# Kernel tuning notes

Measured on AMD Instinct MI355X. Metric: run time of the kernel, lower is better.

Reference implementation:

```python
import jax, jax.numpy as jnp
import numpy as np

N_EMBEDDING = 32
HEAD_SIZE = 64
B, T = 8, 4096


def setup_inputs() -> dict:
    key = jax.random.key(0)
    kx, kk, kq, kv = jax.random.split(key, 4)
    x = jax.random.normal(kx, (B, T, N_EMBEDDING), dtype=jnp.float32)
    Wk = jax.random.normal(kk, (N_EMBEDDING, HEAD_SIZE), dtype=jnp.float32) * 0.05
    Wq = jax.random.normal(kq, (N_EMBEDDING, HEAD_SIZE), dtype=jnp.float32) * 0.05
    Wv = jax.random.normal(kv, (N_EMBEDDING, HEAD_SIZE), dtype=jnp.float32) * 0.05
    return {"x": x, "Wk": Wk, "Wq": Wq, "Wv": Wv}


def reference(x, Wk, Wq, Wv):
    # x: [B, T, C]; projections (no bias)
    k = jnp.einsum("btc,cd->btd", x, Wk)  # [B,T,D]
    q = jnp.einsum("btc,cd->btd", x, Wq)
    v = jnp.einsum("btc,cd->btd", x, Wv)
    # raw scores (NOTE: original module applies no 1/sqrt(D) scaling)
    wei = jnp.einsum("bqd,bkd->bqk", q, k)  # [B,T,T]
    t = x.shape[1]
    causal = jnp.tril(jnp.ones((t, t), dtype=bool))
    wei = jnp.where(causal[None, :, :], wei, -jnp.inf)
    wei = jax.nn.softmax(wei, axis=-1)
    out = jnp.einsum("bqk,bkd->bqd", wei, v)  # [B,T,D]
    return out
```

## Files before the change

### kernel.cpp

```cpp
#include <hip/hip_runtime.h>
#include <hip/hip_bf16.h>

constexpr int Bc = 8;
constexpr int Tt = 4096;
constexpr int Dd = 64;

typedef __attribute__((ext_vector_type(8))) short short8;
typedef __attribute__((ext_vector_type(4))) float floatx4;
typedef __attribute__((ext_vector_type(4))) __fp16 half4;
typedef __attribute__((ext_vector_type(2))) __fp16 half2v;
typedef uint4   __attribute__((may_alias)) uint4_a;
typedef short8  __attribute__((may_alias)) short8_a;
typedef ushort4 __attribute__((may_alias)) ushort4_a;
typedef float4  __attribute__((may_alias)) float4_a;
typedef half4   __attribute__((may_alias)) half4_a;

#define MFMA16(A, B, C)  __builtin_amdgcn_mfma_f32_16x16x32_bf16(A, B, C, 0, 0, 0)
#define MFMAH16(A, B, C) __builtin_amdgcn_mfma_f32_16x16x16f16(A, B, C, 0, 0, 0)
constexpr float LOG2E = 1.4426950408889634f;

__device__ __forceinline__ unsigned rnd16(float x) {
    unsigned u; __builtin_memcpy(&u, &x, 4); return u + 0x8000u;
}
__device__ __forceinline__ unsigned pk_bf2(float lo, float hi) {
    return __builtin_amdgcn_perm(rnd16(hi), rnd16(lo), 0x07060302);
}
__device__ __forceinline__ ushort4 pack4(floatx4 d) {
    union { unsigned u[2]; ushort4 v; } r;
    r.u[0] = pk_bf2(d[0], d[1]);
    r.u[1] = pk_bf2(d[2], d[3]);
    return r.v;
}
__device__ __forceinline__ short8 cvt8(float4 a, float4 b) {
    union { unsigned u[4]; short8 s; } r;
    r.u[0] = pk_bf2(a.x, a.y);
    r.u[1] = pk_bf2(a.z, a.w);
    r.u[2] = pk_bf2(b.x, b.y);
    r.u[3] = pk_bf2(b.z, b.w);
    return r.s;
}

__global__ __launch_bounds__(1024, 4) void attn_kernel(
    const float* __restrict__ x,
    const float* __restrict__ Wk, const float* __restrict__ Wq,
    const float* __restrict__ Wv,
    float* __restrict__ out)
{
    __shared__ uint4 sStage[4096];
    __shared__ uint4 sP[256];
    __shared__ uint4 sG[128];

    int b  = blockIdx.x & 7;
    int pr = blockIdx.x >> 3;
    int tid  = threadIdx.x;
    int wave = tid >> 6, lane = tid & 63;
    int group = wave >> 2, gw = wave & 3;
    int ln15 = lane & 15, quad = lane >> 4;
    size_t bT = (size_t)b * Tt;

    const int tg = tid & 255;
    const int srow = tg >> 2, scg = tg & 3;

    if (wave == 0) {
        floatx4 gC[2][2];
        #pragma unroll
        for (int mt = 0; mt < 2; ++mt)
            #pragma unroll
            for (int nt = 0; nt < 2; ++nt) gC[mt][nt] = (floatx4){0.f,0.f,0.f,0.f};
        #pragma unroll
        for (int kt = 0; kt < 2; ++kt) {
            short8 aG[2], bG[2];
            #pragma unroll
            for (int mt = 0; mt < 2; ++mt) {
                const float* qp = Wq + (ln15 + 16*mt)*64 + 32*kt + quad*8;
                float4 a = ((const float4_a*)qp)[0], bb = ((const float4_a*)qp)[1];
                a.x*=LOG2E; a.y*=LOG2E; a.z*=LOG2E; a.w*=LOG2E;
                bb.x*=LOG2E; bb.y*=LOG2E; bb.z*=LOG2E; bb.w*=LOG2E;
                aG[mt] = cvt8(a, bb);
                const float* kp = Wk + (ln15 + 16*mt)*64 + 32*kt + quad*8;
                bG[mt] = cvt8(((const float4_a*)kp)[0], ((const float4_a*)kp)[1]);
            }
            #pragma unroll
            for (int mt = 0; mt < 2; ++mt)
                #pragma unroll
                for (int nt = 0; nt < 2; ++nt)
                    gC[mt][nt] = MFMA16(aG[mt], bG[nt], gC[mt][nt]);
        }
        unsigned short* sGh = (unsigned short*)sG;
        #pragma unroll
        for (int mt = 0; mt < 2; ++mt)
            #pragma unroll
            for (int nt = 0; nt < 2; ++nt)
                *(ushort4_a*)(sGh + (16*nt + ln15)*32 + 16*mt + quad*4)
                    = pack4(gC[mt][nt]);
    }
    __syncthreads();

    const int gBase = group * 1024;
    unsigned short* sYh = (unsigned short*)sP;

    for (int phase = 0; phase < 2; ++phase) {
        const int qtP = phase ? pr : 63 - pr;
        const int q0 = qtP * 64;
        const int qrow = q0 + gw*16 + ln15;

        float4 pX0, pX1;
        if (group <= qtP) {
            const float* xp = x + (bT + group*64 + srow)*32 + scg*8;
            pX0 = ((const float4_a*)xp)[0];
            pX1 = ((const float4_a*)xp)[1];
        }

        if (wave < 8) {
            int qs = wave & 3, mt = wave >> 2;
            union { uint4 u; short8 s; } g;
            g.u = sG[(16*mt + ln15)*4 + quad];
            const float* xp = x + (bT + q0 + qs*16 + ln15)*32 + quad*8;
            short8 xq = cvt8(((const float4_a*)xp)[0], ((const float4_a*)xp)[1]);
            floatx4 d = (floatx4){0.f,0.f,0.f,0.f};
            d = MFMA16(g.s, xq, d);
            *(ushort4_a*)(sYh + (qs*16 + ln15)*32 + 16*mt + quad*4) = pack4(d);
        }
        __syncthreads();
        short8 bq;
        {
            union { uint4 u; short8 s; } t0;
            t0.u = sP[(gw*16 + ln15)*4 + quad];
            bq = t0.s;
        }

        floatx4 z4[2];
        z4[0] = (floatx4){0.f,0.f,0.f,0.f};
        z4[1] = (floatx4){0.f,0.f,0.f,0.f};
        float l_lane = 0.f;

        const int nIter = (qtP + 4) >> 2;

        for (int it = 0; it < nIter; ++it) {
            int kt = 4*it + group;
            bool active = (kt <= qtP);
            const int stB = gBase + (it & 1) * 512;
            if (active) {
                unsigned u0 = pk_bf2(pX0.x, pX0.y), u1 = pk_bf2(pX0.z, pX0.w);
                unsigned u2 = pk_bf2(pX1.x, pX1.y), u3 = pk_bf2(pX1.z, pX1.w);
                uint4 xu; xu.x = u0; xu.y = u1; xu.z = u2; xu.w = u3;
                sStage[stB + srow*4 + (scg ^ (srow & 3))] = xu;
                union { half2v h; unsigned short us[2]; } w01, w23, w45, w67;
                w01.h = __builtin_amdgcn_cvt_pkrtz(pX0.x, pX0.y);
                w23.h = __builtin_amdgcn_cvt_pkrtz(pX0.z, pX0.w);
                w45.h = __builtin_amdgcn_cvt_pkrtz(pX1.x, pX1.y);
                w67.h = __builtin_amdgcn_cvt_pkrtz(pX1.z, pX1.w);
                unsigned short hv[8] = { w01.us[0], w01.us[1], w23.us[0], w23.us[1],
                                         w45.us[0], w45.us[1], w67.us[0], w67.us[1] };
                unsigned short* sXh = (unsigned short*)(sStage + stB + 256);
                const int cb = scg * 8, gx = srow >> 2, ko = srow & 3;
                #pragma unroll
                for (int jj = 0; jj < 8; ++jj) {
                    int c = cb + jj;
                    sXh[c*64 + ((gx ^ (c & 15)) << 2) + ko] = hv[jj];
                }
            }
            __syncthreads();
            int ktn = kt + 4;
            if (ktn <= qtP) {
                const float* xp = x + (bT + ktn*64 + srow)*32 + scg*8;
                pX0 = ((const float4_a*)xp)[0];
                pX1 = ((const float4_a*)xp)[1];
            }
            if (!active) continue;
            int k0 = kt * 64;

            const int xsw = quad ^ (ln15 & 3);
            floatx4 s4[4];
            #pragma unroll
            for (int t = 0; t < 4; ++t) {
                union { uint4 u; short8 s; } a;
                a.u = sStage[stB + (16*t + ln15)*4 + xsw];
                floatx4 c = (floatx4){0.f,0.f,0.f,0.f};
                c = MFMA16(a.s, bq, c);
                s4[t] = c;
            }

            if (kt == qtP) {
                #pragma unroll
                for (int t = 0; t < 4; ++t) {
                    int keyb = k0 + 16*t + quad*4;
                    #pragma unroll
                    for (int r = 0; r < 4; ++r) {
                        float p = (keyb + r <= qrow) ? __builtin_amdgcn_exp2f(s4[t][r]) : 0.f;
                        s4[t][r] = p;
                        l_lane += p;
                    }
                }
            } else {
                #pragma unroll
                for (int t = 0; t < 4; ++t)
                    #pragma unroll
                    for (int r = 0; r < 4; ++r) {
                        float p = __builtin_amdgcn_exp2f(s4[t][r]);
                        s4[t][r] = p;
                        l_lane += p;
                    }
            }

            const unsigned short* sXh = (const unsigned short*)(sStage + stB + 256);
            #pragma unroll
            for (int t = 0; t < 4; ++t) {
                union { half2v h2[2]; half4 h4; } pb;
                pb.h2[0] = __builtin_amdgcn_cvt_pkrtz(s4[t][0], s4[t][1]);
                pb.h2[1] = __builtin_amdgcn_cvt_pkrtz(s4[t][2], s4[t][3]);
                const int gph = ((4*t + quad) ^ ln15) << 2;
                #pragma unroll
                for (int mt = 0; mt < 2; ++mt) {
                    half4 xa = *(const half4_a*)(sXh + (16*mt + ln15)*64 + gph);
                    z4[mt] = MFMAH16(xa, pb.h4, z4[mt]);
                }
            }
        }

        __syncthreads();
        int li = gw*64 + lane;
        ((float*)sP)[wave*64 + lane] = l_lane;
        if (group != 0) {
            float4* st = (float4*)(sStage + group*1024);
            st[li*2 + 0] = make_float4(z4[0][0], z4[0][1], z4[0][2], z4[0][3]);
            st[li*2 + 1] = make_float4(z4[1][0], z4[1][1], z4[1][2], z4[1][3]);
        }
        __syncthreads();
        if (group == 0) {
            short8 wv_f[4];
            #pragma unroll
            for (int t = 0; t < 4; ++t) {
                int col = 16*t + ln15;
                union { unsigned u[4]; short8 s; } rv;
                #pragma unroll
                for (int jj = 0; jj < 4; ++jj) {
                    const float* v0 = Wv + (quad*8 + 2*jj) * 64 + col;
                    rv.u[jj] = pk_bf2(v0[0], v0[64]);
                }
                wv_f[t] = rv.s;
            }
            float l = l_lane + ((float*)sP)[256 + li]
                    + ((float*)sP)[512 + li] + ((float*)sP)[768 + li];
            l += __shfl_xor(l, 16);
            l += __shfl_xor(l, 32);
            float inv = 1.f / l;
            #pragma unroll
            for (int g = 1; g < 4; ++g) {
                float4* st = (float4*)(sStage + g*1024);
                float4 a = st[li*2 + 0], bb = st[li*2 + 1];
                z4[0][0]+=a.x; z4[0][1]+=a.y; z4[0][2]+=a.z; z4[0][3]+=a.w;
                z4[1][0]+=bb.x; z4[1][1]+=bb.y; z4[1][2]+=bb.z; z4[1][3]+=bb.w;
            }
            unsigned short* sZb = (unsigned short*)sStage;
            #pragma unroll
            for (int mt = 0; mt < 2; ++mt)
                *(ushort4_a*)(sZb + (gw*16 + ln15)*32 + 16*mt + quad*4) = pack4(z4[mt]);
            union { uint4 u; short8 s; } zb;
            zb.u = sStage[(gw*16 + ln15)*4 + quad];
            #pragma unroll
            for (int t = 0; t < 4; ++t) {
                floatx4 o = (floatx4){0.f,0.f,0.f,0.f};
                o = MFMA16(wv_f[t], zb.s, o);
                *(float4_a*)(out + (bT + q0 + gw*16 + ln15)*Dd + 16*t + quad*4)
                    = make_float4(o[0]*inv, o[1]*inv, o[2]*inv, o[3]*inv);
            }
        }
        __syncthreads();
    }
}

extern "C" void kernel_launch(void* const* d_in, const int* in_sizes, int n_in,
                              void* d_out, int out_size, void* d_ws, size_t ws_size,
                              hipStream_t stream)
{
    const float* x  = (const float*)d_in[0];
    const float* Wk = (const float*)d_in[1];
    const float* Wq = (const float*)d_in[2];
    const float* Wv = (const float*)d_in[3];
    float* out = (float*)d_out;

    attn_kernel<<<Bc * 32, 1024, 0, stream>>>(x, Wk, Wq, Wv, out);
}
```

Measured before the change: 86.95 us.

## Process both paired query tiles in one key sweep sharing staged x tiles

Instead of two sequential phases (long tile 63-pr, then short tile pr), the kernel processes both query tiles in a single loop over key tiles, reusing each staged x tile for both score and PV MFMAs. This removes the second pass of x loading, conversion and LDS staging, along with the extra barriers, for the short tile. In exchange it raises register pressure from the doubled accumulators and score arrays, and it doubles the sP buffer.

After: 90.60 us. 4.2% more time.

```diff
diff --git a/kernel.cpp b/kernel.cpp
--- a/kernel.cpp
+++ b/kernel.cpp
@@ -47,11 +47,13 @@
     float* __restrict__ out)
 {
     __shared__ uint4 sStage[4096];
-    __shared__ uint4 sP[256];
+    __shared__ uint4 sP[512];
     __shared__ uint4 sG[128];
 
     int b  = blockIdx.x & 7;
     int pr = blockIdx.x >> 3;
+    const int qtA = 63 - pr, qtB = pr;
+    const int q0A = qtA * 64, q0B = qtB * 64;
     int tid  = threadIdx.x;
     int wave = tid >> 6, lane = tid & 63;
     int group = wave >> 2, gw = wave & 3;
@@ -99,97 +101,117 @@
     const int gBase = group * 1024;
     unsigned short* sYh = (unsigned short*)sP;
 
-    for (int phase = 0; phase < 2; ++phase) {
-        const int qtP = phase ? pr : 63 - pr;
-        const int q0 = qtP * 64;
-        const int qrow = q0 + gw*16 + ln15;
-
-        float4 pX0, pX1;
-        if (group <= qtP) {
-            const float* xp = x + (bT + group*64 + srow)*32 + scg*8;
+    float4 pX0, pX1;
+    {
+        const float* xp = x + (bT + group*64 + srow)*32 + scg*8;
+        pX0 = ((const float4_a*)xp)[0];
+        pX1 = ((const float4_a*)xp)[1];
+    }
+
+    {
+        int tileY = wave >> 3, qs = (wave >> 1) & 3, mt = wave & 1;
+        int q0Y = tileY ? q0B : q0A;
+        union { uint4 u; short8 s; } g;
+        g.u = sG[(16*mt + ln15)*4 + quad];
+        const float* xp = x + (bT + q0Y + qs*16 + ln15)*32 + quad*8;
+        short8 xq = cvt8(((const float4_a*)xp)[0], ((const float4_a*)xp)[1]);
+        floatx4 d = (floatx4){0.f,0.f,0.f,0.f};
+        d = MFMA16(g.s, xq, d);
+        *(ushort4_a*)(sYh + tileY*2048 + (qs*16 + ln15)*32 + 16*mt + quad*4)
+            = pack4(d);
+    }
+    __syncthreads();
+    short8 bqA, bqB;
+    {
+        union { uint4 u; short8 s; } t0, t1;
+        t0.u = sP[(gw*16 + ln15)*4 + quad];
+        t1.u = sP[256 + (gw*16 + ln15)*4 + quad];
+        bqA = t0.s; bqB = t1.s;
+    }
+
+    floatx4 z4A[2], z4B[2];
+    z4A[0] = (floatx4){0.f,0.f,0.f,0.f}; z4A[1] = z4A[0];
+    z4B[0] = z4A[0];                     z4B[1] = z4A[0];
+    float lA = 0.f, lB = 0.f;
+    const int qrowA = q0A + gw*16 + ln15;
+    const int qrowB = q0B + gw*16 + ln15;
+
+    const int nIter = (qtA + 4) >> 2;
+
+    for (int it = 0; it < nIter; ++it) {
+        int kt = 4*it + group;
+        bool activeA = (kt <= qtA);
+        const int stB = gBase + (it & 1) * 512;
+        if (activeA) {
+            unsigned u0 = pk_bf2(pX0.x, pX0.y), u1 = pk_bf2(pX0.z, pX0.w);
+            unsigned u2 = pk_bf2(pX1.x, pX1.y), u3 = pk_bf2(pX1.z, pX1.w);
+            uint4 xu; xu.x = u0; xu.y = u1; xu.z = u2; xu.w = u3;
+            sStage[stB + srow*4 + (scg ^ (srow & 3))] = xu;
+            union { half2v h; unsigned short us[2]; } w01, w23, w45, w67;
+            w01.h = __builtin_amdgcn_cvt_pkrtz(pX0.x, pX0.y);
+            w23.h = __builtin_amdgcn_cvt_pkrtz(pX0.z, pX0.w);
+            w45.h = __builtin_amdgcn_cvt_pkrtz(pX1.x, pX1.y);
+            w67.h = __builtin_amdgcn_cvt_pkrtz(pX1.z, pX1.w);
+            unsigned short hv[8] = { w01.us[0], w01.us[1], w23.us[0], w23.us[1],
+                                     w45.us[0], w45.us[1], w67.us[0], w67.us[1] };
+            unsigned short* sXh = (unsigned short*)(sStage + stB + 256);
+            const int cb = scg * 8, gx = srow >> 2, ko = srow & 3;
+            #pragma unroll
+            for (int jj = 0; jj < 8; ++jj) {
+                int c = cb + jj;
+                sXh[c*64 + ((gx ^ (c & 15)) << 2) + ko] = hv[jj];
+            }
+        }
+        __syncthreads();
+        int ktn = kt + 4;
+        if (ktn <= qtA) {
+            const float* xp = x + (bT + ktn*64 + srow)*32 + scg*8;
             pX0 = ((const float4_a*)xp)[0];
             pX1 = ((const float4_a*)xp)[1];
         }
-
-        if (wave < 8) {
-            int qs = wave & 3, mt = wave >> 2;
-            union { uint4 u; short8 s; } g;
-            g.u = sG[(16*mt + ln15)*4 + quad];
-            const float* xp = x + (bT + q0 + qs*16 + ln15)*32 + quad*8;
-            short8 xq = cvt8(((const float4_a*)xp)[0], ((const float4_a*)xp)[1]);
-            floatx4 d = (floatx4){0.f,0.f,0.f,0.f};
-            d = MFMA16(g.s, xq, d);
-            *(ushort4_a*)(sYh + (qs*16 + ln15)*32 + 16*mt + quad*4) = pack4(d);
-        }
-        __syncthreads();
-        short8 bq;
-        {
-            union { uint4 u; short8 s; } t0;
-            t0.u = sP[(gw*16 + ln15)*4 + quad];
-            bq = t0.s;
-        }
-
-        floatx4 z4[2];
-        z4[0] = (floatx4){0.f,0.f,0.f,0.f};
-        z4[1] = (floatx4){0.f,0.f,0.f,0.f};
-        float l_lane = 0.f;
-
-        const int nIter = (qtP + 4) >> 2;
-
-        for (int it = 0; it < nIter; ++it) {
-            int kt = 4*it + group;
-            bool active = (kt <= qtP);
-            const int stB = gBase + (it & 1) * 512;
-            if (active) {
-                unsigned u0 = pk_bf2(pX0.x, pX0.y), u1 = pk_bf2(pX0.z, pX0.w);
-                unsigned u2 = pk_bf2(pX1.x, pX1.y), u3 = pk_bf2(pX1.z, pX1.w);
-                uint4 xu; xu.x = u0; xu.y = u1; xu.z = u2; xu.w = u3;
-                sStage[stB + srow*4 + (scg ^ (srow & 3))] = xu;
-                union { half2v h; unsigned short us[2]; } w01, w23, w45, w67;
-                w01.h = __builtin_amdgcn_cvt_pkrtz(pX0.x, pX0.y);
-                w23.h = __builtin_amdgcn_cvt_pkrtz(pX0.z, pX0.w);
-                w45.h = __builtin_amdgcn_cvt_pkrtz(pX1.x, pX1.y);
-                w67.h = __builtin_amdgcn_cvt_pkrtz(pX1.z, pX1.w);
-                unsigned short hv[8] = { w01.us[0], w01.us[1], w23.us[0], w23.us[1],
-                                         w45.us[0], w45.us[1], w67.us[0], w67.us[1] };
-                unsigned short* sXh = (unsigned short*)(sStage + stB + 256);
-                const int cb = scg * 8, gx = srow >> 2, ko = srow & 3;
-                #pragma unroll
-                for (int jj = 0; jj < 8; ++jj) {
-                    int c = cb + jj;
-                    sXh[c*64 + ((gx ^ (c & 15)) << 2) + ko] = hv[jj];
+        if (!activeA) continue;
+        int k0 = kt * 64;
+        bool doB = (kt <= qtB);
+
+        const int xsw = quad ^ (ln15 & 3);
+        floatx4 sA[4], sB[4];
+        #pragma unroll
+        for (int t = 0; t < 4; ++t) {
+            union { uint4 u; short8 s; } a;
+            a.u = sStage[stB + (16*t + ln15)*4 + xsw];
+            floatx4 c = (floatx4){0.f,0.f,0.f,0.f};
+            sA[t] = MFMA16(a.s, bqA, c);
+            if (doB) sB[t] = MFMA16(a.s, bqB, c);
+        }
+
+        if (kt == qtA) {
+            #pragma unroll
+            for (int t = 0; t < 4; ++t) {
+                int keyb = k0 + 16*t + quad*4;
+                #pragma unroll
+                for (int r = 0; r < 4; ++r) {
+                    float p = (keyb + r <= qrowA) ? __builtin_amdgcn_exp2f(sA[t][r]) : 0.f;
+                    sA[t][r] = p; lA += p;
                 }
             }
-            __syncthreads();
-            int ktn = kt + 4;
-            if (ktn <= qtP) {
-                const float* xp = x + (bT + ktn*64 + srow)*32 + scg*8;
-                pX0 = ((const float4_a*)xp)[0];
-                pX1 = ((const float4_a*)xp)[1];
-            }
-            if (!active) continue;
-            int k0 = kt * 64;
-
-            const int xsw = quad ^ (ln15 & 3);
-            floatx4 s4[4];
-            #pragma unroll
-            for (int t = 0; t < 4; ++t) {
-                union { uint4 u; short8 s; } a;
-                a.u = sStage[stB + (16*t + ln15)*4 + xsw];
-                floatx4 c = (floatx4){0.f,0.f,0.f,0.f};
-                c = MFMA16(a.s, bq, c);
-                s4[t] = c;
-            }
-
-            if (kt == qtP) {
+        } else {
+            #pragma unroll
+            for (int t = 0; t < 4; ++t)
+                #pragma unroll
+                for (int r = 0; r < 4; ++r) {
+                    float p = __builtin_amdgcn_exp2f(sA[t][r]);
+                    sA[t][r] = p; lA += p;
+                }
+        }
+        if (doB) {
+            if (kt == qtB) {
                 #pragma unroll
                 for (int t = 0; t < 4; ++t) {
                     int keyb = k0 + 16*t + quad*4;
                     #pragma unroll
                     for (int r = 0; r < 4; ++r) {
-                        float p = (keyb + r <= qrow) ? __builtin_amdgcn_exp2f(s4[t][r]) : 0.f;
-                        s4[t][r] = p;
-                        l_lane += p;
+                        float p = (keyb + r <= qrowB) ? __builtin_amdgcn_exp2f(sB[t][r]) : 0.f;
+                        sB[t][r] = p; lB += p;
                     }
                 }
             } else {
@@ -197,76 +219,89 @@
                 for (int t = 0; t < 4; ++t)
                     #pragma unroll
                     for (int r = 0; r < 4; ++r) {
-                        float p = __builtin_amdgcn_exp2f(s4[t][r]);
-                        s4[t][r] = p;
-                        l_lane += p;
+                        float p = __builtin_amdgcn_exp2f(sB[t][r]);
+                        sB[t][r] = p; lB += p;
                     }
             }
-
-            const unsigned short* sXh = (const unsigned short*)(sStage + stB + 256);
-            #pragma unroll
-            for (int t = 0; t < 4; ++t) {
-                union { half2v h2[2]; half4 h4; } pb;
-                pb.h2[0] = __builtin_amdgcn_cvt_pkrtz(s4[t][0], s4[t][1]);
-                pb.h2[1] = __builtin_amdgcn_cvt_pkrtz(s4[t][2], s4[t][3]);
-                const int gph = ((4*t + quad) ^ ln15) << 2;
-                #pragma unroll
-                for (int mt = 0; mt < 2; ++mt) {
-                    half4 xa = *(const half4_a*)(sXh + (16*mt + ln15)*64 + gph);
-                    z4[mt] = MFMAH16(xa, pb.h4, z4[mt]);
-                }
-            }
-        }
-
-        __syncthreads();
-        int li = gw*64 + lane;
-        ((float*)sP)[wave*64 + lane] = l_lane;
-        if (group != 0) {
-            float4* st = (float4*)(sStage + group*1024);
-            st[li*2 + 0] = make_float4(z4[0][0], z4[0][1], z4[0][2], z4[0][3]);
-            st[li*2 + 1] = make_float4(z4[1][0], z4[1][1], z4[1][2], z4[1][3]);
-        }
-        __syncthreads();
-        if (group == 0) {
-            short8 wv_f[4];
-            #pragma unroll
-            for (int t = 0; t < 4; ++t) {
-                int col = 16*t + ln15;
-                union { unsigned u[4]; short8 s; } rv;
-                #pragma unroll
-                for (int jj = 0; jj < 4; ++jj) {
-                    const float* v0 = Wv + (quad*8 + 2*jj) * 64 + col;
-                    rv.u[jj] = pk_bf2(v0[0], v0[64]);
-                }
-                wv_f[t] = rv.s;
-            }
-            float l = l_lane + ((float*)sP)[256 + li]
-                    + ((float*)sP)[512 + li] + ((float*)sP)[768 + li];
+        }
+
+        const unsigned short* sXh = (const unsigned short*)(sStage + stB + 256);
+        #pragma unroll
+        for (int t = 0; t < 4; ++t) {
+            union { half2v h2[2]; half4 h4; } pA, pB;
+            pA.h2[0] = __builtin_amdgcn_cvt_pkrtz(sA[t][0], sA[t][1]);
+            pA.h2[1] = __builtin_amdgcn_cvt_pkrtz(sA[t][2], sA[t][3]);
+            if (doB) {
+                pB.h2[0] = __builtin_amdgcn_cvt_pkrtz(sB[t][0], sB[t][1]);
+                pB.h2[1] = __builtin_amdgcn_cvt_pkrtz(sB[t][2], sB[t][3]);
+            }
+            const int gph = ((4*t + quad) ^ ln15) << 2;
+            #pragma unroll
+            for (int mt = 0; mt < 2; ++mt) {
+                half4 xa = *(const half4_a*)(sXh + (16*mt + ln15)*64 + gph);
+                z4A[mt] = MFMAH16(xa, pA.h4, z4A[mt]);
+                if (doB) z4B[mt] = MFMAH16(xa, pB.h4, z4B[mt]);
+            }
+        }
+    }
+
+    __syncthreads();
+    int li = gw*64 + lane;
+    ((float*)sP)[wave*64 + lane] = lA;
+    ((float*)sP)[1024 + wave*64 + lane] = lB;
+    if (group != 0) {
+        float4* st = (float4*)(sStage + group*1024);
+        st[li*2 + 0] = make_float4(z4A[0][0], z4A[0][1], z4A[0][2], z4A[0][3]);
+        st[li*2 + 1] = make_float4(z4A[1][0], z4A[1][1], z4A[1][2], z4A[1][3]);
+        st[512 + li*2 + 0] = make_float4(z4B[0][0], z4B[0][1], z4B[0][2], z4B[0][3]);
+        st[512 + li*2 + 1] = make_float4(z4B[1][0], z4B[1][1], z4B[1][2], z4B[1][3]);
+    }
+    __syncthreads();
+    if (group == 0) {
+        short8 wv_f[4];
+        #pragma unroll
+        for (int t = 0; t < 4; ++t) {
+            int col = 16*t + ln15;
+            union { unsigned u[4]; short8 s; } rv;
+            #pragma unroll
+            for (int jj = 0; jj < 4; ++jj) {
+                const float* v0 = Wv + (quad*8 + 2*jj) * 64 + col;
+                rv.u[jj] = pk_bf2(v0[0], v0[64]);
+            }
+            wv_f[t] = rv.s;
+        }
+        unsigned short* sZb = (unsigned short*)sStage;
+        #pragma unroll
+        for (int tile = 0; tile < 2; ++tile) {
+            floatx4* z4 = tile ? z4B : z4A;
+            int lofs = tile * 1024, sofs = tile * 512;
+            float l = ((float*)sP)[lofs + li] + ((float*)sP)[lofs + 256 + li]
+                    + ((float*)sP)[lofs + 512 + li] + ((float*)sP)[lofs + 768 + li];
             l += __shfl_xor(l, 16);
             l += __shfl_xor(l, 32);
             float inv = 1.f / l;
             #pragma unroll
             for (int g = 1; g < 4; ++g) {
                 float4* st = (float4*)(sStage + g*1024);
-                float4 a = st[li*2 + 0], bb = st[li*2 + 1];
+                float4 a = st[sofs + li*2 + 0], bb = st[sofs + li*2 + 1];
                 z4[0][0]+=a.x; z4[0][1]+=a.y; z4[0][2]+=a.z; z4[0][3]+=a.w;
                 z4[1][0]+=bb.x; z4[1][1]+=bb.y; z4[1][2]+=bb.z; z4[1][3]+=bb.w;
             }
-            unsigned short* sZb = (unsigned short*)sStage;
             #pragma unroll
             for (int mt = 0; mt < 2; ++mt)
-                *(ushort4_a*)(sZb + (gw*16 + ln15)*32 + 16*mt + quad*4) = pack4(z4[mt]);
+                *(ushort4_a*)(sZb + tile*2048 + (gw*16 + ln15)*32 + 16*mt + quad*4)
+                    = pack4(z4[mt]);
             union { uint4 u; short8 s; } zb;
-            zb.u = sStage[(gw*16 + ln15)*4 + quad];
+            zb.u = sStage[tile*256 + (gw*16 + ln15)*4 + quad];
+            int q0T = tile ? q0B : q0A;
             #pragma unroll
             for (int t = 0; t < 4; ++t) {
                 floatx4 o = (floatx4){0.f,0.f,0.f,0.f};
                 o = MFMA16(wv_f[t], zb.s, o);
-                *(float4_a*)(out + (bT + q0 + gw*16 + ln15)*Dd + 16*t + quad*4)
+                *(float4_a*)(out + (bT + q0T + gw*16 + ln15)*Dd + 16*t + quad*4)
                     = make_float4(o[0]*inv, o[1]*inv, o[2]*inv, o[3]*inv);
             }
         }
-        __syncthreads();
     }
 }
 
```

## Split work into one query tile per 512-thread block with two key groups

Applied to the files above, without the earlier changes.

Each block previously used 1024 threads in four key-split groups and handled a pair of query tiles, one long and one short, to balance causal work. Now each 512-thread block handles a single query tile with two key-split groups, and the grid doubles to 512 blocks, launched from the heaviest tile downward. This halves shared memory and the cross-group reduction, and puts more independent blocks on the device. It also fuses the exp and fp16 pack into the score loop, which lowers register pressure. The risk is load imbalance across blocks of very different lengths and fewer waves per block to hide latency.

Result: slower. 92.49 us (+6.4%).

```diff
diff --git a/kernel.cpp b/kernel.cpp
--- a/kernel.cpp
+++ b/kernel.cpp
@@ -40,18 +40,19 @@
     return r.s;
 }
 
-__global__ __launch_bounds__(1024, 4) void attn_kernel(
+__global__ __launch_bounds__(512, 4) void attn_kernel(
     const float* __restrict__ x,
     const float* __restrict__ Wk, const float* __restrict__ Wq,
     const float* __restrict__ Wv,
     float* __restrict__ out)
 {
-    __shared__ uint4 sStage[4096];
+    __shared__ uint4 sStage[2048];
     __shared__ uint4 sP[256];
     __shared__ uint4 sG[128];
 
-    int b  = blockIdx.x & 7;
-    int pr = blockIdx.x >> 3;
+    int b   = blockIdx.x & 7;
+    int qt  = 63 - (blockIdx.x >> 3);
+    const int q0 = qt * 64;
     int tid  = threadIdx.x;
     int wave = tid >> 6, lane = tid & 63;
     int group = wave >> 2, gw = wave & 3;
@@ -99,174 +100,159 @@
     const int gBase = group * 1024;
     unsigned short* sYh = (unsigned short*)sP;
 
-    for (int phase = 0; phase < 2; ++phase) {
-        const int qtP = phase ? pr : 63 - pr;
-        const int q0 = qtP * 64;
-        const int qrow = q0 + gw*16 + ln15;
-
-        float4 pX0, pX1;
-        if (group <= qtP) {
-            const float* xp = x + (bT + group*64 + srow)*32 + scg*8;
+    float4 pX0, pX1;
+    if (group <= qt) {
+        const float* xp = x + (bT + group*64 + srow)*32 + scg*8;
+        pX0 = ((const float4_a*)xp)[0];
+        pX1 = ((const float4_a*)xp)[1];
+    }
+
+    {
+        int qs = wave & 3, mt = (wave >> 2) & 1;
+        union { uint4 u; short8 s; } g;
+        g.u = sG[(16*mt + ln15)*4 + quad];
+        const float* xp = x + (bT + q0 + qs*16 + ln15)*32 + quad*8;
+        short8 xq = cvt8(((const float4_a*)xp)[0], ((const float4_a*)xp)[1]);
+        floatx4 d = (floatx4){0.f,0.f,0.f,0.f};
+        d = MFMA16(g.s, xq, d);
+        *(ushort4_a*)(sYh + (qs*16 + ln15)*32 + 16*mt + quad*4) = pack4(d);
+    }
+    __syncthreads();
+    short8 bq;
+    {
+        union { uint4 u; short8 s; } t0;
+        t0.u = sP[(gw*16 + ln15)*4 + quad];
+        bq = t0.s;
+    }
+
+    floatx4 z4[2];
+    z4[0] = (floatx4){0.f,0.f,0.f,0.f};
+    z4[1] = z4[0];
+    float l_lane = 0.f;
+    const int qrow = q0 + gw*16 + ln15;
+
+    const int nIter = (qt + 2) >> 1;
+
+    for (int it = 0; it < nIter; ++it) {
+        int kt = 2*it + group;
+        bool active = (kt <= qt);
+        const int stB = gBase + (it & 1) * 512;
+        if (active) {
+            unsigned u0 = pk_bf2(pX0.x, pX0.y), u1 = pk_bf2(pX0.z, pX0.w);
+            unsigned u2 = pk_bf2(pX1.x, pX1.y), u3 = pk_bf2(pX1.z, pX1.w);
+            uint4 xu; xu.x = u0; xu.y = u1; xu.z = u2; xu.w = u3;
+            sStage[stB + srow*4 + (scg ^ (srow & 3))] = xu;
+            union { half2v h; unsigned short us[2]; } w01, w23, w45, w67;
+            w01.h = __builtin_amdgcn_cvt_pkrtz(pX0.x, pX0.y);
+            w23.h = __builtin_amdgcn_cvt_pkrtz(pX0.z, pX0.w);
+            w45.h = __builtin_amdgcn_cvt_pkrtz(pX1.x, pX1.y);
+            w67.h = __builtin_amdgcn_cvt_pkrtz(pX1.z, pX1.w);
+            unsigned short hv[8] = { w01.us[0], w01.us[1], w23.us[0], w23.us[1],
+                                     w45.us[0], w45.us[1], w67.us[0], w67.us[1] };
+            unsigned short* sXh = (unsigned short*)(sStage + stB + 256);
+            const int cb = scg * 8, gx = srow >> 2, ko = srow & 3;
+            #pragma unroll
+            for (int jj = 0; jj < 8; ++jj) {
+                int c = cb + jj;
+                sXh[c*64 + ((gx ^ (c & 15)) << 2) + ko] = hv[jj];
+            }
+        }
+        __syncthreads();
+        int ktn = kt + 2;
+        if (ktn <= qt) {
+            const float* xp = x + (bT + ktn*64 + srow)*32 + scg*8;
             pX0 = ((const float4_a*)xp)[0];
             pX1 = ((const float4_a*)xp)[1];
         }
-
-        if (wave < 8) {
-            int qs = wave & 3, mt = wave >> 2;
-            union { uint4 u; short8 s; } g;
-            g.u = sG[(16*mt + ln15)*4 + quad];
-            const float* xp = x + (bT + q0 + qs*16 + ln15)*32 + quad*8;
-            short8 xq = cvt8(((const float4_a*)xp)[0], ((const float4_a*)xp)[1]);
-            floatx4 d = (floatx4){0.f,0.f,0.f,0.f};
-            d = MFMA16(g.s, xq, d);
-            *(ushort4_a*)(sYh + (qs*16 + ln15)*32 + 16*mt + quad*4) = pack4(d);
-        }
-        __syncthreads();
-        short8 bq;
+        if (!active) continue;
+        int k0 = kt * 64;
+        const bool diag = (kt == qt);
+
+        const int xsw = quad ^ (ln15 & 3);
+        half4 pA[4];
+        #pragma unroll
+        for (int t = 0; t < 4; ++t) {
+            union { uint4 u; short8 s; } a;
+            a.u = sStage[stB + (16*t + ln15)*4 + xsw];
+            const int keyb = k0 + 16*t + quad*4;
+            floatx4 cz = (floatx4){0.f,0.f,0.f,0.f};
+            floatx4 s = MFMA16(a.s, bq, cz);
+            float p0, p1, p2, p3;
+            if (diag) {
+                p0 = (keyb + 0 <= qrow) ? __builtin_amdgcn_exp2f(s[0]) : 0.f;
+                p1 = (keyb + 1 <= qrow) ? __builtin_amdgcn_exp2f(s[1]) : 0.f;
+                p2 = (keyb + 2 <= qrow) ? __builtin_amdgcn_exp2f(s[2]) : 0.f;
+                p3 = (keyb + 3 <= qrow) ? __builtin_amdgcn_exp2f(s[3]) : 0.f;
+            } else {
+                p0 = __builtin_amdgcn_exp2f(s[0]);
+                p1 = __builtin_amdgcn_exp2f(s[1]);
+                p2 = __builtin_amdgcn_exp2f(s[2]);
+                p3 = __builtin_amdgcn_exp2f(s[3]);
+            }
+            l_lane += p0 + p1 + p2 + p3;
+            union { half2v h2[2]; half4 h4; } u;
+            u.h2[0] = __builtin_amdgcn_cvt_pkrtz(p0, p1);
+            u.h2[1] = __builtin_amdgcn_cvt_pkrtz(p2, p3);
+            pA[t] = u.h4;
+        }
+
+        const unsigned short* sXh = (const unsigned short*)(sStage + stB + 256);
+        #pragma unroll
+        for (int t = 0; t < 4; ++t) {
+            const int gph = ((4*t + quad) ^ ln15) << 2;
+            #pragma unroll
+            for (int mt = 0; mt < 2; ++mt) {
+                half4 xa = *(const half4_a*)(sXh + (16*mt + ln15)*64 + gph);
+                z4[mt] = MFMAH16(xa, pA[t], z4[mt]);
+            }
+        }
+    }
+
+    __syncthreads();
+    int li = gw*64 + lane;
+    ((float*)sP)[wave*64 + lane] = l_lane;
+    if (group == 1) {
+        float4* st = (float4*)(sStage + 1024);
+        st[li*2 + 0] = make_float4(z4[0][0], z4[0][1], z4[0][2], z4[0][3]);
+        st[li*2 + 1] = make_float4(z4[1][0], z4[1][1], z4[1][2], z4[1][3]);
+    }
+    __syncthreads();
+    if (group == 0) {
+        short8 wv_f[4];
+        #pragma unroll
+        for (int t = 0; t < 4; ++t) {
+            int col = 16*t + ln15;
+            union { unsigned u[4]; short8 s; } rv;
+            #pragma unroll
+            for (int jj = 0; jj < 4; ++jj) {
+                const float* v0 = Wv + (quad*8 + 2*jj) * 64 + col;
+                rv.u[jj] = pk_bf2(v0[0], v0[64]);
+            }
+            wv_f[t] = rv.s;
+        }
+        float l = ((float*)sP)[li] + ((float*)sP)[256 + li];
+        l += __shfl_xor(l, 16);
+        l += __shfl_xor(l, 32);
+        float inv = 1.f / l;
         {
-            union { uint4 u; short8 s; } t0;
-            t0.u = sP[(gw*16 + ln15)*4 + quad];
-            bq = t0.s;
-        }
-
-        floatx4 z4[2];
-        z4[0] = (floatx4){0.f,0.f,0.f,0.f};
-        z4[1] = (floatx4){0.f,0.f,0.f,0.f};
-        float l_lane = 0.f;
-
-        const int nIter = (qtP + 4) >> 2;
-
-        for (int it = 0; it < nIter; ++it) {
-            int kt = 4*it + group;
-            bool active = (kt <= qtP);
-            const int stB = gBase + (it & 1) * 512;
-            if (active) {
-                unsigned u0 = pk_bf2(pX0.x, pX0.y), u1 = pk_bf2(pX0.z, pX0.w);
-                unsigned u2 = pk_bf2(pX1.x, pX1.y), u3 = pk_bf2(pX1.z, pX1.w);
-                uint4 xu; xu.x = u0; xu.y = u1; xu.z = u2; xu.w = u3;
-                sStage[stB + srow*4 + (scg ^ (srow & 3))] = xu;
-                union { half2v h; unsigned short us[2]; } w01, w23, w45, w67;
-                w01.h = __builtin_amdgcn_cvt_pkrtz(pX0.x, pX0.y);
-                w23.h = __builtin_amdgcn_cvt_pkrtz(pX0.z, pX0.w);
-                w45.h = __builtin_amdgcn_cvt_pkrtz(pX1.x, pX1.y);
-                w67.h = __builtin_amdgcn_cvt_pkrtz(pX1.z, pX1.w);
-                unsigned short hv[8] = { w01.us[0], w01.us[1], w23.us[0], w23.us[1],
-                                         w45.us[0], w45.us[1], w67.us[0], w67.us[1] };
-                unsigned short* sXh = (unsigned short*)(sStage + stB + 256);
-                const int cb = scg * 8, gx = srow >> 2, ko = srow & 3;
-                #pragma unroll
-                for (int jj = 0; jj < 8; ++jj) {
-                    int c = cb + jj;
-                    sXh[c*64 + ((gx ^ (c & 15)) << 2) + ko] = hv[jj];
-                }
-            }
-            __syncthreads();
-            int ktn = kt + 4;
-            if (ktn <= qtP) {
-                const float* xp = x + (bT + ktn*64 + srow)*32 + scg*8;
-                pX0 = ((const float4_a*)xp)[0];
-                pX1 = ((const float4_a*)xp)[1];
-            }
-            if (!active) continue;
-            int k0 = kt * 64;
-
-            const int xsw = quad ^ (ln15 & 3);
-            floatx4 s4[4];
-            #pragma unroll
-            for (int t = 0; t < 4; ++t) {
-                union { uint4 u; short8 s; } a;
-                a.u = sStage[stB + (16*t + ln15)*4 + xsw];
-                floatx4 c = (floatx4){0.f,0.f,0.f,0.f};
-                c = MFMA16(a.s, bq, c);
-                s4[t] = c;
-            }
-
-            if (kt == qtP) {
-                #pragma unroll
-                for (int t = 0; t < 4; ++t) {
-                    int keyb = k0 + 16*t + quad*4;
-                    #pragma unroll
-                    for (int r = 0; r < 4; ++r) {
-                        float p = (keyb + r <= qrow) ? __builtin_amdgcn_exp2f(s4[t][r]) : 0.f;
-                        s4[t][r] = p;
-                        l_lane += p;
-                    }
-                }
-            } else {
-                #pragma unroll
-                for (int t = 0; t < 4; ++t)
-                    #pragma unroll
-                    for (int r = 0; r < 4; ++r) {
-                        float p = __builtin_amdgcn_exp2f(s4[t][r]);
-                        s4[t][r] = p;
-                        l_lane += p;
-                    }
-            }
-
-            const unsigned short* sXh = (const unsigned short*)(sStage + stB + 256);
-            #pragma unroll
-            for (int t = 0; t < 4; ++t) {
-                union { half2v h2[2]; half4 h4; } pb;
-                pb.h2[0] = __builtin_amdgcn_cvt_pkrtz(s4[t][0], s4[t][1]);
-                pb.h2[1] = __builtin_amdgcn_cvt_pkrtz(s4[t][2], s4[t][3]);
-                const int gph = ((4*t + quad) ^ ln15) << 2;
-                #pragma unroll
-                for (int mt = 0; mt < 2; ++mt) {
-                    half4 xa = *(const half4_a*)(sXh + (16*mt + ln15)*64 + gph);
-                    z4[mt] = MFMAH16(xa, pb.h4, z4[mt]);
-                }
-            }
-        }
-
-        __syncthreads();
-        int li = gw*64 + lane;
-        ((float*)sP)[wave*64 + lane] = l_lane;
-        if (group != 0) {
-            float4* st = (float4*)(sStage + group*1024);
-            st[li*2 + 0] = make_float4(z4[0][0], z4[0][1], z4[0][2], z4[0][3]);
-            st[li*2 + 1] = make_float4(z4[1][0], z4[1][1], z4[1][2], z4[1][3]);
-        }
-        __syncthreads();
-        if (group == 0) {
-            short8 wv_f[4];
-            #pragma unroll
-            for (int t = 0; t < 4; ++t) {
-                int col = 16*t + ln15;
-                union { unsigned u[4]; short8 s; } rv;
-                #pragma unroll
-                for (int jj = 0; jj < 4; ++jj) {
-                    const float* v0 = Wv + (quad*8 + 2*jj) * 64 + col;
-                    rv.u[jj] = pk_bf2(v0[0], v0[64]);
-                }
-                wv_f[t] = rv.s;
-            }
-            float l = l_lane + ((float*)sP)[256 + li]
-                    + ((float*)sP)[512 + li] + ((float*)sP)[768 + li];
-            l += __shfl_xor(l, 16);
-            l += __shfl_xor(l, 32);
-            float inv = 1.f / l;
-            #pragma unroll
-            for (int g = 1; g < 4; ++g) {
-                float4* st = (float4*)(sStage + g*1024);
-                float4 a = st[li*2 + 0], bb = st[li*2 + 1];
-                z4[0][0]+=a.x; z4[0][1]+=a.y; z4[0][2]+=a.z; z4[0][3]+=a.w;
-                z4[1][0]+=bb.x; z4[1][1]+=bb.y; z4[1][2]+=bb.z; z4[1][3]+=bb.w;
-            }
-            unsigned short* sZb = (unsigned short*)sStage;
-            #pragma unroll
-            for (int mt = 0; mt < 2; ++mt)
-                *(ushort4_a*)(sZb + (gw*16 + ln15)*32 + 16*mt + quad*4) = pack4(z4[mt]);
-            union { uint4 u; short8 s; } zb;
-            zb.u = sStage[(gw*16 + ln15)*4 + quad];
-            #pragma unroll
-            for (int t = 0; t < 4; ++t) {
-                floatx4 o = (floatx4){0.f,0.f,0.f,0.f};
-                o = MFMA16(wv_f[t], zb.s, o);
-                *(float4_a*)(out + (bT + q0 + gw*16 + ln15)*Dd + 16*t + quad*4)
-                    = make_float4(o[0]*inv, o[1]*inv, o[2]*inv, o[3]*inv);
-            }
-        }
-        __syncthreads();
+            float4* st = (float4*)(sStage + 1024);
+            float4 a = st[li*2 + 0], bb = st[li*2 + 1];
+            z4[0][0]+=a.x; z4[0][1]+=a.y; z4[0][2]+=a.z; z4[0][3]+=a.w;
+            z4[1][0]+=bb.x; z4[1][1]+=bb.y; z4[1][2]+=bb.z; z4[1][3]+=bb.w;
+        }
+        unsigned short* sZb = (unsigned short*)sStage;
+        #pragma unroll
+        for (int mt = 0; mt < 2; ++mt)
+            *(ushort4_a*)(sZb + (gw*16 + ln15)*32 + 16*mt + quad*4) = pack4(z4[mt]);
+        union { uint4 u; short8 s; } zb;
+        zb.u = sStage[(gw*16 + ln15)*4 + quad];
+        #pragma unroll
+        for (int t = 0; t < 4; ++t) {
+            floatx4 o = (floatx4){0.f,0.f,0.f,0.f};
+            o = MFMA16(wv_f[t], zb.s, o);
+            *(float4_a*)(out + (bT + q0 + gw*16 + ln15)*Dd + 16*t + quad*4)
+                = make_float4(o[0]*inv, o[1]*inv, o[2]*inv, o[3]*inv);
+        }
     }
 }
 
@@ -280,5 +266,5 @@
     const float* Wv = (const float*)d_in[3];
     float* out = (float*)d_out;
 
-    attn_kernel<<<Bc * 32, 1024, 0, stream>>>(x, Wk, Wq, Wv, out);
-}
+    attn_kernel<<<Bc * 64, 512, 0, stream>>>(x, Wk, Wq, Wv, out);
+}
```
